# Performance work log

Measured on AMD Instinct MI355X. Metric: run time of the kernel, lower is better.

## Reference

```python
import jax, jax.numpy as jnp
import numpy as np

OBS_LEN = 20
IN_DIM = 64
HID_DIM = 128
BATCH = 65536


def setup_inputs() -> dict:
    key = jax.random.key(0)
    ks = jax.random.split(key, 9)
    s_emb = 1.0 / np.sqrt(2.0)
    s_lstm = 1.0 / np.sqrt(HID_DIM)
    return {
        "obs_goal": jax.random.normal(ks[0], (OBS_LEN, BATCH, 2), dtype=jnp.float32),
        "h0": jax.random.normal(ks[1], (BATCH, HID_DIM), dtype=jnp.float32),
        "c0": jax.random.normal(ks[2], (BATCH, HID_DIM), dtype=jnp.float32),
        "W_emb": jax.random.uniform(ks[3], (IN_DIM, 2), jnp.float32, -s_emb, s_emb),
        "b_emb": jax.random.uniform(ks[4], (IN_DIM,), jnp.float32, -s_emb, s_emb),
        "W_ih": jax.random.uniform(ks[5], (4 * HID_DIM, IN_DIM), jnp.float32, -s_lstm, s_lstm),
        "W_hh": jax.random.uniform(ks[6], (4 * HID_DIM, HID_DIM), jnp.float32, -s_lstm, s_lstm),
        "b_ih": jax.random.uniform(ks[7], (4 * HID_DIM,), jnp.float32, -s_lstm, s_lstm),
        "b_hh": jax.random.uniform(ks[8], (4 * HID_DIM,), jnp.float32, -s_lstm, s_lstm),
    }


def reference(obs_goal, h0, c0, W_emb, b_emb, W_ih, W_hh, b_ih, b_hh):
    # input embedding: [T*B, 2] @ [2, D] -> [T, B, D]
    T, B, _ = obs_goal.shape
    x_emb = (obs_goal.reshape(-1, 2) @ W_emb.T + b_emb).reshape(T, B, IN_DIM)

    def step(carry, x_t):
        h, c = carry
        # gates: [B, 4H], torch LSTMCell chunk order = (i, f, g, o)
        gates = x_t @ W_ih.T + b_ih + h @ W_hh.T + b_hh
        i, f, g, o = jnp.split(gates, 4, axis=-1)
        i = jax.nn.sigmoid(i)
        f = jax.nn.sigmoid(f)
        g = jnp.tanh(g)
        o = jax.nn.sigmoid(o)
        c_new = f * c + i * g
        h_new = o * jnp.tanh(c_new)
        return (h_new, c_new), None

    (h_final, _), _ = jax.lax.scan(step, (h0, c0), x_emb[:OBS_LEN])
    return h_final
```

## Files before the change

### kernel.cpp

```cpp
#include <hip/hip_runtime.h>

#define OBS_T 20
#define HID 128
#define NGATE 512
#define MB 16
#define HSTR 136

typedef __bf16 bf16x8 __attribute__((ext_vector_type(8)));
typedef __bf16 bf16x4 __attribute__((ext_vector_type(4)));
typedef float f32x4 __attribute__((ext_vector_type(4)));
typedef float f32x2 __attribute__((ext_vector_type(2)));

__device__ __forceinline__ float fast_rcp(float x) { return __builtin_amdgcn_rcpf(x); }
#if __has_builtin(__builtin_amdgcn_exp2f)
__device__ __forceinline__ float exp2_hw(float x) { return __builtin_amdgcn_exp2f(x); }
#else
__device__ __forceinline__ float exp2_hw(float x) { return __expf(x * 0.69314718056f); }
#endif
#define LOG2E 1.442695041f

__device__ __host__ __forceinline__ float gate_scale(int q) {
  return (q == 2) ? (-2.0f * LOG2E) : (-LOG2E);
}

__global__ void prep_vec(const float* __restrict__ W_emb, const float* __restrict__ b_emb,
                         const float* __restrict__ W_ih, const float* __restrict__ b_ih,
                         const float* __restrict__ b_hh,
                         float* __restrict__ biasp, float* __restrict__ wx0p,
                         float* __restrict__ wx1p) {
  int r = blockIdx.x * blockDim.x + threadIdx.x;
  if (r >= NGATE) return;
  float s0 = 0.f, s1 = 0.f, sb = 0.f;
  for (int d = 0; d < 64; ++d) {
    float w = W_ih[r * 64 + d];
    s0 += w * W_emb[d * 2 + 0];
    s1 += w * W_emb[d * 2 + 1];
    sb += w * b_emb[d];
  }
  int q = r >> 7, j = r & 127;
  float sc = gate_scale(q);
  int np = (j >> 4) * 64 + q * 16 + (j & 15);
  biasp[np] = (b_ih[r] + b_hh[r] + sb) * sc;
  wx0p[np] = s0 * sc;
  wx1p[np] = s1 * sc;
}

__global__ void prep_wp(const float* __restrict__ W_hh, __bf16* __restrict__ Wp) {
  int tid = blockIdx.x * blockDim.x + threadIdx.x;
  int jj = tid & 7;
  int lane = (tid >> 3) & 63;
  int frag = tid >> 9;
  int ks = frag & 3;
  int q = (frag >> 2) & 3;
  int g16 = frag >> 4;
  int cn = lane & 15, quad = lane >> 4;
  int r = q * 128 + g16 * 16 + cn;
  int k = ks * 32 + quad * 8 + jj;
  Wp[tid] = (__bf16)(W_hh[r * 128 + k] * gate_scale(q));
}

__device__ __forceinline__ f32x2 exp2_2(f32x2 v) {
  f32x2 r;
  r.x = exp2_hw(v.x);
  r.y = exp2_hw(v.y);
  return r;
}
__device__ __forceinline__ f32x2 rcp_2(f32x2 v) {
  f32x2 r;
  r.x = fast_rcp(v.x);
  r.y = fast_rcp(v.y);
  return r;
}

__device__ __forceinline__ f32x2 cell_update_pk(f32x2 gi, f32x2 gf, f32x2 gg,
                                                f32x2 go, f32x2& c) {
  f32x2 e_i = exp2_2(gi);
  f32x2 e_f = exp2_2(gf);
  f32x2 e_g = exp2_2(gg);
  f32x2 e_o = exp2_2(go);
  f32x2 a_i = e_i + 1.f;
  f32x2 a_f = e_f + 1.f;
  f32x2 a_g = e_g + 1.f;
  f32x2 bg = 1.f - e_g;
  f32x2 m1 = a_i * a_g;
  f32x2 r = rcp_2(m1 * a_f);
  f32x2 t = c * m1 + bg * a_f;
  c = t * r;
  f32x2 e_c = exp2_2(c * (-2.f * LOG2E));
  f32x2 a_c = e_c + 1.f;
  f32x2 bc = 1.f - e_c;
  return bc * rcp_2((e_o + 1.f) * a_c);
}

__global__ __launch_bounds__(256, 2) void lstm_fused(
    const float* __restrict__ obs, const float* __restrict__ h0,
    const float* __restrict__ c0, const __bf16* __restrict__ Wp,
    const float* __restrict__ biasp, const float* __restrict__ wx0p,
    const float* __restrict__ wx1p, float* __restrict__ out, int batch) {
  __shared__ __align__(16) __bf16 hbuf[2][MB][HSTR];
  __shared__ __align__(16) float obs_s[OBS_T][MB][2];
  __shared__ __align__(16) float wx0_s[NGATE];
  __shared__ __align__(16) float wx1_s[NGATE];

  const int tid = threadIdx.x;
  const int lane = tid & 63;
  const int wv = tid >> 6;
  const int cn = lane & 15;
  const int quad = lane >> 4;
  const int bbase = blockIdx.x * MB;
  const int ju0 = (wv * 2) * 16 + cn;

  if (tid < OBS_T * MB * 2 / 4) {
    const int t = tid >> 3, f4 = tid & 7;
    ((float4*)obs_s)[tid] = ((const float4*)obs)[(t * batch + bbase) / 2 + f4];
  }
#pragma unroll
  for (int it = 0; it < 2; ++it) {
    int i = tid + it * 256;
    wx0_s[i] = wx0p[i];
    wx1_s[i] = wx1p[i];
  }
#pragma unroll
  for (int it = 0; it < 2; ++it) {
    int idx = tid + it * 256;
    int row = idx >> 5, c4 = idx & 31;
    float4 v = ((const float4*)h0)[(bbase + row) * 32 + c4];
    bf16x4 b;
    b.x = (__bf16)v.x; b.y = (__bf16)v.y; b.z = (__bf16)v.z; b.w = (__bf16)v.w;
    *(bf16x4*)&hbuf[0][row][c4 * 4] = b;
  }

  bf16x8 Bf[2][4][4];
  {
    const bf16x8* wp8 = (const bf16x8*)Wp;
#pragma unroll
    for (int u = 0; u < 2; ++u)
#pragma unroll
      for (int q = 0; q < 4; ++q)
#pragma unroll
        for (int ks = 0; ks < 4; ++ks)
          Bf[u][ks][q] = wp8[((wv * 2 + u) * 16 + q * 4 + ks) * 64 + lane];
  }

  float bias_v[2][4];
#pragma unroll
  for (int u = 0; u < 2; ++u)
#pragma unroll
    for (int q = 0; q < 4; ++q)
      bias_v[u][q] = biasp[(wv * 2 + u) * 64 + q * 16 + cn];

  f32x2 cc2[2][2];
#pragma unroll
  for (int u = 0; u < 2; ++u)
#pragma unroll
    for (int p = 0; p < 2; ++p) {
      int ju = ju0 + u * 16;
      cc2[u][p].x = c0[(bbase + quad * 4 + 2 * p + 0) * HID + ju];
      cc2[u][p].y = c0[(bbase + quad * 4 + 2 * p + 1) * HID + ju];
    }

  __syncthreads();

  int cur = 0;
#pragma unroll 1
  for (int t = 0; t < OBS_T - 1; ++t) {
    f32x4 acc[2][4];
#pragma unroll
    for (int u = 0; u < 2; ++u)
#pragma unroll
      for (int q = 0; q < 4; ++q) {
        int n = (wv * 2 + u) * 64 + q * 16 + cn;
        float w0q = wx0_s[n], w1q = wx1_s[n];
#pragma unroll
        for (int r = 0; r < 4; ++r) {
          float2 ob = *(const float2*)&obs_s[t][quad * 4 + r][0];
          acc[u][q][r] = fmaf(ob.y, w1q, fmaf(ob.x, w0q, bias_v[u][q]));
        }
      }

#pragma unroll
    for (int ks = 0; ks < 4; ++ks) {
      bf16x8 Av = *(const bf16x8*)&hbuf[cur][cn][ks * 32 + quad * 8];
#pragma unroll
      for (int q = 0; q < 4; ++q) {
        acc[0][q] = __builtin_amdgcn_mfma_f32_16x16x32_bf16(Av, Bf[0][ks][q], acc[0][q], 0, 0, 0);
        acc[1][q] = __builtin_amdgcn_mfma_f32_16x16x32_bf16(Av, Bf[1][ks][q], acc[1][q], 0, 0, 0);
      }
    }

    const int nxt = cur ^ 1;
#pragma unroll
    for (int u = 0; u < 2; ++u) {
      const int ju = ju0 + u * 16;
      f32x2 hlo = cell_update_pk(acc[u][0].xy, acc[u][1].xy, acc[u][2].xy,
                                 acc[u][3].xy, cc2[u][0]);
      f32x2 hhi = cell_update_pk(acc[u][0].zw, acc[u][1].zw, acc[u][2].zw,
                                 acc[u][3].zw, cc2[u][1]);
      hbuf[nxt][quad * 4 + 0][ju] = (__bf16)hlo.x;
      hbuf[nxt][quad * 4 + 1][ju] = (__bf16)hlo.y;
      hbuf[nxt][quad * 4 + 2][ju] = (__bf16)hhi.x;
      hbuf[nxt][quad * 4 + 3][ju] = (__bf16)hhi.y;
    }
    __syncthreads();
    cur = nxt;
  }

  {
    const int t = OBS_T - 1;
    f32x4 acc[2][4];
#pragma unroll
    for (int u = 0; u < 2; ++u)
#pragma unroll
      for (int q = 0; q < 4; ++q) {
        int n = (wv * 2 + u) * 64 + q * 16 + cn;
        float w0q = wx0_s[n], w1q = wx1_s[n];
#pragma unroll
        for (int r = 0; r < 4; ++r) {
          float2 ob = *(const float2*)&obs_s[t][quad * 4 + r][0];
          acc[u][q][r] = fmaf(ob.y, w1q, fmaf(ob.x, w0q, bias_v[u][q]));
        }
      }
#pragma unroll
    for (int ks = 0; ks < 4; ++ks) {
      bf16x8 Av = *(const bf16x8*)&hbuf[cur][cn][ks * 32 + quad * 8];
#pragma unroll
      for (int q = 0; q < 4; ++q) {
        acc[0][q] = __builtin_amdgcn_mfma_f32_16x16x32_bf16(Av, Bf[0][ks][q], acc[0][q], 0, 0, 0);
        acc[1][q] = __builtin_amdgcn_mfma_f32_16x16x32_bf16(Av, Bf[1][ks][q], acc[1][q], 0, 0, 0);
      }
    }
#pragma unroll
    for (int u = 0; u < 2; ++u) {
      const int ju = ju0 + u * 16;
      f32x2 hlo = cell_update_pk(acc[u][0].xy, acc[u][1].xy, acc[u][2].xy,
                                 acc[u][3].xy, cc2[u][0]);
      f32x2 hhi = cell_update_pk(acc[u][0].zw, acc[u][1].zw, acc[u][2].zw,
                                 acc[u][3].zw, cc2[u][1]);
      out[(bbase + quad * 4 + 0) * HID + ju] = hlo.x;
      out[(bbase + quad * 4 + 1) * HID + ju] = hlo.y;
      out[(bbase + quad * 4 + 2) * HID + ju] = hhi.x;
      out[(bbase + quad * 4 + 3) * HID + ju] = hhi.y;
    }
  }
}

extern "C" void kernel_launch(void* const* d_in, const int* in_sizes, int n_in,
                              void* d_out, int out_size, void* d_ws, size_t ws_size,
                              hipStream_t stream) {
  const float* obs = (const float*)d_in[0];
  const float* h0 = (const float*)d_in[1];
  const float* c0 = (const float*)d_in[2];
  const float* W_emb = (const float*)d_in[3];
  const float* b_emb = (const float*)d_in[4];
  const float* W_ih = (const float*)d_in[5];
  const float* W_hh = (const float*)d_in[6];
  const float* b_ih = (const float*)d_in[7];
  const float* b_hh = (const float*)d_in[8];
  float* out = (float*)d_out;
  const int batch = in_sizes[1] / HID;

  __bf16* Wp = (__bf16*)d_ws;
  float* biasp = (float*)((char*)d_ws + 131072);
  float* wx0p = biasp + NGATE;
  float* wx1p = wx0p + NGATE;

  prep_vec<<<2, 256, 0, stream>>>(W_emb, b_emb, W_ih, b_ih, b_hh, biasp, wx0p, wx1p);
  prep_wp<<<256, 256, 0, stream>>>(W_hh, Wp);
  lstm_fused<<<batch / MB, 256, 0, stream>>>(obs, h0, c0, Wp, biasp, wx0p, wx1p, out, batch);
}
```

Before: 336.6 us.

## Split LSTM gate columns across eight waves per block instead of four

The block grows from 256 to 512 threads, and each wave now owns 16 hidden units (64 gate columns) rather than 32, halving the per-thread MFMA work, weight registers and cell-update work per timestep. The aim is shorter per-step latency on the serial recurrence and more waves per CU to hide MFMA and transcendental latency, with launch bounds raised to 512x4. In exchange the per-step __syncthreads spans twice as many waves, and each wave issues the same hbuf A-fragment LDS reads for fewer MFMAs.

```diff
diff --git a/kernel.cpp b/kernel.cpp
--- a/kernel.cpp
+++ b/kernel.cpp
@@ -92,7 +92,7 @@
   return bc * rcp_2((e_o + 1.f) * a_c);
 }
 
-__global__ __launch_bounds__(256, 2) void lstm_fused(
+__global__ __launch_bounds__(512, 4) void lstm_fused(
     const float* __restrict__ obs, const float* __restrict__ h0,
     const float* __restrict__ c0, const __bf16* __restrict__ Wp,
     const float* __restrict__ biasp, const float* __restrict__ wx0p,
@@ -108,94 +108,73 @@
   const int cn = lane & 15;
   const int quad = lane >> 4;
   const int bbase = blockIdx.x * MB;
-  const int ju0 = (wv * 2) * 16 + cn;
+  const int ju = wv * 16 + cn;
 
   if (tid < OBS_T * MB * 2 / 4) {
     const int t = tid >> 3, f4 = tid & 7;
     ((float4*)obs_s)[tid] = ((const float4*)obs)[(t * batch + bbase) / 2 + f4];
   }
-#pragma unroll
-  for (int it = 0; it < 2; ++it) {
-    int i = tid + it * 256;
-    wx0_s[i] = wx0p[i];
-    wx1_s[i] = wx1p[i];
-  }
-#pragma unroll
-  for (int it = 0; it < 2; ++it) {
-    int idx = tid + it * 256;
-    int row = idx >> 5, c4 = idx & 31;
+  wx0_s[tid] = wx0p[tid];
+  wx1_s[tid] = wx1p[tid];
+  {
+    int row = tid >> 5, c4 = tid & 31;
     float4 v = ((const float4*)h0)[(bbase + row) * 32 + c4];
     bf16x4 b;
     b.x = (__bf16)v.x; b.y = (__bf16)v.y; b.z = (__bf16)v.z; b.w = (__bf16)v.w;
     *(bf16x4*)&hbuf[0][row][c4 * 4] = b;
   }
 
-  bf16x8 Bf[2][4][4];
+  bf16x8 Bf[4][4];
   {
     const bf16x8* wp8 = (const bf16x8*)Wp;
 #pragma unroll
-    for (int u = 0; u < 2; ++u)
-#pragma unroll
-      for (int q = 0; q < 4; ++q)
-#pragma unroll
-        for (int ks = 0; ks < 4; ++ks)
-          Bf[u][ks][q] = wp8[((wv * 2 + u) * 16 + q * 4 + ks) * 64 + lane];
-  }
-
-  float bias_v[2][4];
-#pragma unroll
-  for (int u = 0; u < 2; ++u)
-#pragma unroll
     for (int q = 0; q < 4; ++q)
-      bias_v[u][q] = biasp[(wv * 2 + u) * 64 + q * 16 + cn];
-
-  f32x2 cc2[2][2];
-#pragma unroll
-  for (int u = 0; u < 2; ++u)
-#pragma unroll
-    for (int p = 0; p < 2; ++p) {
-      int ju = ju0 + u * 16;
-      cc2[u][p].x = c0[(bbase + quad * 4 + 2 * p + 0) * HID + ju];
-      cc2[u][p].y = c0[(bbase + quad * 4 + 2 * p + 1) * HID + ju];
-    }
+#pragma unroll
+      for (int ks = 0; ks < 4; ++ks)
+        Bf[ks][q] = wp8[(wv * 16 + q * 4 + ks) * 64 + lane];
+  }
+
+  float bias_v[4];
+#pragma unroll
+  for (int q = 0; q < 4; ++q)
+    bias_v[q] = biasp[wv * 64 + q * 16 + cn];
+
+  f32x2 cc2[2];
+#pragma unroll
+  for (int p = 0; p < 2; ++p) {
+    cc2[p].x = c0[(bbase + quad * 4 + 2 * p + 0) * HID + ju];
+    cc2[p].y = c0[(bbase + quad * 4 + 2 * p + 1) * HID + ju];
+  }
 
   __syncthreads();
 
   int cur = 0;
 #pragma unroll 1
   for (int t = 0; t < OBS_T - 1; ++t) {
-    f32x4 acc[2][4];
-#pragma unroll
-    for (int u = 0; u < 2; ++u)
-#pragma unroll
-      for (int q = 0; q < 4; ++q) {
-        int n = (wv * 2 + u) * 64 + q * 16 + cn;
-        float w0q = wx0_s[n], w1q = wx1_s[n];
-#pragma unroll
-        for (int r = 0; r < 4; ++r) {
-          float2 ob = *(const float2*)&obs_s[t][quad * 4 + r][0];
-          acc[u][q][r] = fmaf(ob.y, w1q, fmaf(ob.x, w0q, bias_v[u][q]));
-        }
+    f32x4 acc[4];
+#pragma unroll
+    for (int q = 0; q < 4; ++q) {
+      int n = wv * 64 + q * 16 + cn;
+      float w0q = wx0_s[n], w1q = wx1_s[n];
+#pragma unroll
+      for (int r = 0; r < 4; ++r) {
+        float2 ob = *(const float2*)&obs_s[t][quad * 4 + r][0];
+        acc[q][r] = fmaf(ob.y, w1q, fmaf(ob.x, w0q, bias_v[q]));
       }
+    }
 
 #pragma unroll
     for (int ks = 0; ks < 4; ++ks) {
       bf16x8 Av = *(const bf16x8*)&hbuf[cur][cn][ks * 32 + quad * 8];
 #pragma unroll
-      for (int q = 0; q < 4; ++q) {
-        acc[0][q] = __builtin_amdgcn_mfma_f32_16x16x32_bf16(Av, Bf[0][ks][q], acc[0][q], 0, 0, 0);
-        acc[1][q] = __builtin_amdgcn_mfma_f32_16x16x32_bf16(Av, Bf[1][ks][q], acc[1][q], 0, 0, 0);
-      }
+      for (int q = 0; q < 4; ++q)
+        acc[q] = __builtin_amdgcn_mfma_f32_16x16x32_bf16(Av, Bf[ks][q], acc[q], 0, 0, 0);
     }
 
     const int nxt = cur ^ 1;
-#pragma unroll
-    for (int u = 0; u < 2; ++u) {
-      const int ju = ju0 + u * 16;
-      f32x2 hlo = cell_update_pk(acc[u][0].xy, acc[u][1].xy, acc[u][2].xy,
-                                 acc[u][3].xy, cc2[u][0]);
-      f32x2 hhi = cell_update_pk(acc[u][0].zw, acc[u][1].zw, acc[u][2].zw,
-                                 acc[u][3].zw, cc2[u][1]);
+    {
+      f32x2 hlo = cell_update_pk(acc[0].xy, acc[1].xy, acc[2].xy, acc[3].xy, cc2[0]);
+      f32x2 hhi = cell_update_pk(acc[0].zw, acc[1].zw, acc[2].zw, acc[3].zw, cc2[1]);
       hbuf[nxt][quad * 4 + 0][ju] = (__bf16)hlo.x;
       hbuf[nxt][quad * 4 + 1][ju] = (__bf16)hlo.y;
       hbuf[nxt][quad * 4 + 2][ju] = (__bf16)hhi.x;
@@ -207,35 +186,27 @@
 
   {
     const int t = OBS_T - 1;
-    f32x4 acc[2][4];
-#pragma unroll
-    for (int u = 0; u < 2; ++u)
-#pragma unroll
-      for (int q = 0; q < 4; ++q) {
-        int n = (wv * 2 + u) * 64 + q * 16 + cn;
-        float w0q = wx0_s[n], w1q = wx1_s[n];
-#pragma unroll
-        for (int r = 0; r < 4; ++r) {
-          float2 ob = *(const float2*)&obs_s[t][quad * 4 + r][0];
-          acc[u][q][r] = fmaf(ob.y, w1q, fmaf(ob.x, w0q, bias_v[u][q]));
-        }
+    f32x4 acc[4];
+#pragma unroll
+    for (int q = 0; q < 4; ++q) {
+      int n = wv * 64 + q * 16 + cn;
+      float w0q = wx0_s[n], w1q = wx1_s[n];
+#pragma unroll
+      for (int r = 0; r < 4; ++r) {
+        float2 ob = *(const float2*)&obs_s[t][quad * 4 + r][0];
+        acc[q][r] = fmaf(ob.y, w1q, fmaf(ob.x, w0q, bias_v[q]));
       }
+    }
 #pragma unroll
     for (int ks = 0; ks < 4; ++ks) {
       bf16x8 Av = *(const bf16x8*)&hbuf[cur][cn][ks * 32 + quad * 8];
 #pragma unroll
-      for (int q = 0; q < 4; ++q) {
-        acc[0][q] = __builtin_amdgcn_mfma_f32_16x16x32_bf16(Av, Bf[0][ks][q], acc[0][q], 0, 0, 0);
-        acc[1][q] = __builtin_amdgcn_mfma_f32_16x16x32_bf16(Av, Bf[1][ks][q], acc[1][q], 0, 0, 0);
-      }
-    }
-#pragma unroll
-    for (int u = 0; u < 2; ++u) {
-      const int ju = ju0 + u * 16;
-      f32x2 hlo = cell_update_pk(acc[u][0].xy, acc[u][1].xy, acc[u][2].xy,
-                                 acc[u][3].xy, cc2[u][0]);
-      f32x2 hhi = cell_update_pk(acc[u][0].zw, acc[u][1].zw, acc[u][2].zw,
-                                 acc[u][3].zw, cc2[u][1]);
+      for (int q = 0; q < 4; ++q)
+        acc[q] = __builtin_amdgcn_mfma_f32_16x16x32_bf16(Av, Bf[ks][q], acc[q], 0, 0, 0);
+    }
+    {
+      f32x2 hlo = cell_update_pk(acc[0].xy, acc[1].xy, acc[2].xy, acc[3].xy, cc2[0]);
+      f32x2 hhi = cell_update_pk(acc[0].zw, acc[1].zw, acc[2].zw, acc[3].zw, cc2[1]);
       out[(bbase + quad * 4 + 0) * HID + ju] = hlo.x;
       out[(bbase + quad * 4 + 1) * HID + ju] = hlo.y;
       out[(bbase + quad * 4 + 2) * HID + ju] = hhi.x;
@@ -266,5 +237,5 @@
 
   prep_vec<<<2, 256, 0, stream>>>(W_emb, b_emb, W_ih, b_ih, b_hh, biasp, wx0p, wx1p);
   prep_wp<<<256, 256, 0, stream>>>(W_hh, Wp);
-  lstm_fused<<<batch / MB, 256, 0, stream>>>(obs, h0, c0, Wp, biasp, wx0p, wx1p, out, batch);
-}
+  lstm_fused<<<batch / MB, 512, 0, stream>>>(obs, h0, c0, Wp, biasp, wx0p, wx1p, out, batch);
+}
```

Result: slower. 348.9 us (+3.7%).
